# Kernel tuning notes

Hardware: AMD Instinct MI355X
Metric: run time of the kernel (lower is better)

Reference implementation:

```python
import jax, jax.numpy as jnp
import numpy as np

B, N, D, H, HID, EN = 2, 4096, 128, 4, 32, 16
ALPHA = 0.2           # LeakyReLU slope
NEG = -9e15           # masked_fill value from the original code


def setup_inputs() -> dict:
    key = jax.random.key(0)
    ks = jax.random.split(key, 6)
    fea = jax.random.normal(ks[0], (B, N, D), dtype=jnp.float32)
    # binary dense adjacency (regulon x gene), square here so narrow() is identity
    adj = jax.random.randint(ks[1], (B, N, N), 0, 2).astype(jnp.float32)
    # per-head GAT params (xavier-ish scale)
    W_heads = jax.random.normal(ks[2], (H, D, HID), dtype=jnp.float32) * 0.1
    a_heads = jax.random.normal(ks[3], (H, 2 * HID, 1), dtype=jnp.float32) * 0.1
    W_last = jax.random.normal(ks[4], (H * HID, EN), dtype=jnp.float32) * 0.1
    a_last = jax.random.normal(ks[5], (2 * EN, 1), dtype=jnp.float32) * 0.1
    return {"fea_mats": fea, "adj_mats": adj, "W_heads": W_heads,
            "a_heads": a_heads, "W_last": W_last, "a_last": a_last}


def _gat_layer(x, adj, W, a, concat):
    # x: [N, d_in], adj: [nr, N], W: [d_in, out], a: [2*out, 1]
    out_dim = W.shape[1]
    wh = x @ W                                   # [N, out]
    nr = adj.shape[0]
    wh1 = wh[:nr] @ a[:out_dim]                  # [nr, 1]
    wh2 = wh @ a[out_dim:]                       # [N, 1]
    e = jax.nn.leaky_relu(wh1 + wh2.T, ALPHA)    # [nr, N]
    # _prepare_attentions: mask by adj, weight by adj, fill zeros with -9e15
    att = jnp.where(adj != 0, e * adj, 0.0)
    att = jnp.where(att == 0, NEG, att)
    att = jax.nn.softmax(att, axis=1)
    # the original detaches attention via a numpy roundtrip
    att = jax.lax.stop_gradient(att)
    res = att @ wh                               # [nr, out]
    return jax.nn.elu(res) if concat else res


def reference(fea_mats, adj_mats, W_heads, a_heads, W_last, a_last):
    def per_sample(x, adj):
        # multi-head attention layers (concat=True), vmapped over heads
        heads = jax.vmap(lambda W, a: _gat_layer(x, adj, W, a, True))(W_heads, a_heads)  # [H, N, HID]
        xcat = jnp.transpose(heads, (1, 0, 2)).reshape(x.shape[0], H * HID)  # torch.cat(dim=1)
        nr = adj.shape[0]
        out = _gat_layer(xcat, adj[:, :nr], W_last, a_last, False)  # adj.narrow(1,0,nr)
        return jax.nn.elu(out)  # [N, EN]
    return jax.vmap(per_sample)(fea_mats, adj_mats)  # [B, N, EN]
```

## Files before the change

### kernel.cpp

```cpp
#include <hip/hip_runtime.h>
#include <hip/hip_bf16.h>
#include <stdint.h>

#define B_ 2
#define N_ 4096
#define D_ 128
#define H_ 4
#define HID_ 32
#define EN_ 16
#define ALPHA_ 0.2f
#define S1_ 4
#define S2_ 4
#define LOG2E_ 1.4426950408889634f

typedef __attribute__((ext_vector_type(8))) _Float16 f16x8;
typedef __attribute__((ext_vector_type(4))) float f32x4;
typedef __attribute__((ext_vector_type(8))) unsigned short u16x8;

__device__ __forceinline__ unsigned short f2h(float v) {
    _Float16 h = (_Float16)v;
    return *(unsigned short*)&h;
}

__global__ __launch_bounds__(256) void prep_kernel(
    const float* __restrict__ adj, unsigned long long* __restrict__ mask,
    const float* __restrict__ fea, const float* __restrict__ Wh,
    const float* __restrict__ a_heads,
    float* __restrict__ wh1, float* __restrict__ wh2,
    float* __restrict__ cmax1, unsigned short* __restrict__ whTt)
{
    __shared__ float xs[32][132];
    __shared__ float WT[32][132];
    __shared__ float Wa[2][128];
    __shared__ float as_[2 * HID_];
    __shared__ unsigned short ts[32][32];
    __shared__ float rmax[32];
    const int tid = threadIdx.x;

    if (blockIdx.x < 2048) {
        const int b = blockIdx.x >> 10, ib = blockIdx.x & 1023;
        const int i = ib * 4 + (tid >> 6);
        const int lane = tid & 63;
        const float* ar = adj + ((size_t)b * N_ + i) * N_;
        unsigned long long* mrow = mask + ((size_t)b * N_ + i) * 64;
#pragma unroll 4
        for (int c = 0; c < 16; ++c) {
            float4 v = *(const float4*)(ar + c * 256 + lane * 4);
            unsigned long long b0 = __ballot(v.x != 0.f);
            unsigned long long b1 = __ballot(v.y != 0.f);
            unsigned long long b2 = __ballot(v.z != 0.f);
            unsigned long long b3 = __ballot(v.w != 0.f);
            if (lane == 0) {
                ulonglong2 w01 = {b0, b1}, w23 = {b2, b3};
                *(ulonglong2*)(mrow + c * 4) = w01;
                *(ulonglong2*)(mrow + c * 4 + 2) = w23;
            }
        }
        return;
    }
    const int l0 = blockIdx.x - 2048;
    const int ib = l0 & 127, h = (l0 >> 7) & 3, b = l0 >> 9;
    const int i0 = ib * 32;
    const float* Wp = Wh + (size_t)h * D_ * HID_;
    for (int l = tid; l < 1024; l += 256) {
        float4 w4 = *(const float4*)(Wp + l * 4);
        int k = l >> 3, d = (l & 7) * 4;
        WT[d][k] = w4.x; WT[d + 1][k] = w4.y; WT[d + 2][k] = w4.z; WT[d + 3][k] = w4.w;
    }
    if (tid < 2 * HID_) as_[tid] = a_heads[h * 2 * HID_ + tid];
    const float* xp = fea + ((size_t)b * N_ + i0) * D_;
    for (int l = tid; l < 1024; l += 256) {
        int r = l >> 5, k4 = (l & 31) * 4;
        *(float4*)&xs[r][k4] = *(const float4*)(xp + r * D_ + k4);
    }
    __syncthreads();
    {
        const int k = tid & 127, j = tid >> 7;
        const float* wr = Wp + k * HID_;
        const float* aw = &as_[j * HID_];
        float s = 0.f;
#pragma unroll
        for (int d = 0; d < HID_; d += 4) {
            float4 w4 = *(const float4*)(wr + d);
            s += w4.x * aw[d] + w4.y * aw[d + 1] + w4.z * aw[d + 2] + w4.w * aw[d + 3];
        }
        Wa[j][k] = s;
    }
    const int c = tid & 15, rg = (tid >> 4) * 2;
    float a0[2] = {0.f, 0.f}, a1[2] = {0.f, 0.f};
#pragma unroll 8
    for (int k = 0; k < D_; k += 4) {
        float4 w0 = *(float4*)&WT[c][k];
        float4 w1 = *(float4*)&WT[c + 16][k];
#pragma unroll
        for (int i = 0; i < 2; ++i) {
            float4 x4 = *(float4*)&xs[rg + i][k];
            a0[i] += x4.x * w0.x + x4.y * w0.y + x4.z * w0.z + x4.w * w0.w;
            a1[i] += x4.x * w1.x + x4.y * w1.y + x4.z * w1.z + x4.w * w1.w;
        }
    }
#pragma unroll
    for (int i = 0; i < 2; ++i) {
        ts[c][rg + i] = f2h(a0[i]);
        ts[c + 16][rg + i] = f2h(a1[i]);
    }
    __syncthreads();
    {
        const int row = tid >> 3, q = tid & 7;
        float d1 = 0.f, d2 = 0.f;
#pragma unroll
        for (int k = q * 16; k < q * 16 + 16; k += 4) {
            float4 x4 = *(float4*)&xs[row][k];
            float4 u = *(float4*)&Wa[0][k];
            float4 v = *(float4*)&Wa[1][k];
            d1 += x4.x * u.x + x4.y * u.y + x4.z * u.z + x4.w * u.w;
            d2 += x4.x * v.x + x4.y * v.y + x4.z * v.z + x4.w * v.w;
        }
        d1 += __shfl_xor(d1, 1); d1 += __shfl_xor(d1, 2); d1 += __shfl_xor(d1, 4);
        d2 += __shfl_xor(d2, 1); d2 += __shfl_xor(d2, 2); d2 += __shfl_xor(d2, 4);
        if (q == 0) {
            const size_t o = (size_t)(b * H_ + h) * N_ + i0 + row;
            wh1[o] = d1 * LOG2E_;
            wh2[o] = d2 * LOG2E_;
            rmax[row] = d2 * LOG2E_;
        }
    }
    __syncthreads();
    if (tid < 128) {
        const int d = tid >> 2, part = (tid & 3) * 8;
        unsigned short* dst = whTt + ((size_t)(b * H_ + h) * 64 + (i0 >> 6)) * 2048
                            + d * 64 + (i0 & 63) + part;
        *(u16x8*)dst = *(u16x8*)&ts[d][part];
    }
    if (tid < 32) {
        float mx = rmax[tid];
#pragma unroll
        for (int off = 16; off; off >>= 1) mx = fmaxf(mx, __shfl_xor(mx, off));
        if (tid == 0) cmax1[(size_t)(b * H_ + h) * 128 + ib] = mx;
    }
}

__global__ __launch_bounds__(256) void attn1_kernel(
    const unsigned long long* __restrict__ mask, const unsigned short* __restrict__ whT,
    const float* __restrict__ wh1, const float* __restrict__ wh2,
    const float* __restrict__ cmax1,
    float* __restrict__ x2p, float* __restrict__ l1p)
{
    __shared__ unsigned long long mask_s[32][17];
    __shared__ float Btab[H_][2][1024];
    const int b = blockIdx.z, split = blockIdx.y, i0 = blockIdx.x * 32;
    const int tid = threadIdx.x, lane = tid & 63, h = tid >> 6;
    const int m = lane & 15, quad = lane >> 4;
    {
        const int r = tid >> 3, w = (tid & 7) * 2;
        ulonglong2 mw = *(const ulonglong2*)(mask + ((size_t)b * N_ + i0 + r) * 64
                                             + split * 16 + w);
        mask_s[r][w] = mw.x; mask_s[r][w + 1] = mw.y;
    }
    const float* cm = cmax1 + (size_t)(b * H_ + h) * 128;
    float Mh = fmaxf(cm[lane], cm[lane + 64]);
#pragma unroll
    for (int off = 32; off; off >>= 1) Mh = fmaxf(Mh, __shfl_xor(Mh, off));
    const size_t bhN = (size_t)(b * H_ + h) * N_;
    const float* w2g = wh2 + bhN + split * 1024;
#pragma unroll
    for (int g = 0; g < 4; ++g) {
        float4 v = *(const float4*)(w2g + g * 256 + lane * 4);
        float4 eb, ep;
        eb.x = __builtin_amdgcn_exp2f(v.x - Mh);
        eb.y = __builtin_amdgcn_exp2f(v.y - Mh);
        eb.z = __builtin_amdgcn_exp2f(v.z - Mh);
        eb.w = __builtin_amdgcn_exp2f(v.w - Mh);
        ep.x = __builtin_amdgcn_exp2f(ALPHA_ * (v.x - Mh));
        ep.y = __builtin_amdgcn_exp2f(ALPHA_ * (v.y - Mh));
        ep.z = __builtin_amdgcn_exp2f(ALPHA_ * (v.z - Mh));
        ep.w = __builtin_amdgcn_exp2f(ALPHA_ * (v.w - Mh));
        *(float4*)&Btab[h][0][g * 256 + lane * 4] = eb;
        *(float4*)&Btab[h][1][g * 256 + lane * 4] = ep;
    }
    const float w1r0 = wh1[bhN + i0 + m];
    const float w1r1 = wh1[bhN + i0 + 16 + m];
    const float sb0 = w1r0 + Mh, sb1 = w1r1 + Mh;
    const float mr0 = fmaxf(sb0, ALPHA_ * sb0);
    const float mr1 = fmaxf(sb1, ALPHA_ * sb1);
    const float th0 = -w1r0, th1 = -w1r1;
    const float Fp0 = __builtin_amdgcn_exp2f(sb0 - mr0);
    const float Fn0 = __builtin_amdgcn_exp2f(ALPHA_ * sb0 - mr0);
    const float Fp1 = __builtin_amdgcn_exp2f(sb1 - mr1);
    const float Fn1 = __builtin_amdgcn_exp2f(ALPHA_ * sb1 - mr1);
    const float* wvb = wh2 + bhN + split * 1024 + quad * 8;
    const unsigned short* bpb = whT + (size_t)(b * H_ + h) * 131072
                              + (size_t)split * 16 * 2048 + m * 64 + quad * 8;
    f32x4 a00 = {0.f,0.f,0.f,0.f}, a01 = {0.f,0.f,0.f,0.f}, a02 = {0.f,0.f,0.f,0.f};
    f32x4 a10 = {0.f,0.f,0.f,0.f}, a11 = {0.f,0.f,0.f,0.f}, a12 = {0.f,0.f,0.f,0.f};
    f16x8 ones;
#pragma unroll
    for (int q = 0; q < 8; ++q) ones[q] = (_Float16)1.0f;
    __syncthreads();

    for (int c = 0; c < 4; ++c) {
#pragma unroll
        for (int q4 = 0; q4 < 4; ++q4) {
            const int t = c * 4 + q4;
            const int half = q4 >> 1;
            unsigned int pw0, pw1, pw2, pw3, qw0, qw1, qw2, qw3;
            pw0 = ((const unsigned int*)&mask_s[m][c*4+0])[half];
            pw1 = ((const unsigned int*)&mask_s[m][c*4+1])[half];
            pw2 = ((const unsigned int*)&mask_s[m][c*4+2])[half];
            pw3 = ((const unsigned int*)&mask_s[m][c*4+3])[half];
            qw0 = ((const unsigned int*)&mask_s[m+16][c*4+0])[half];
            qw1 = ((const unsigned int*)&mask_s[m+16][c*4+1])[half];
            qw2 = ((const unsigned int*)&mask_s[m+16][c*4+2])[half];
            qw3 = ((const unsigned int*)&mask_s[m+16][c*4+3])[half];
            const unsigned short* bp = bpb + (size_t)t * 2048;
            const float* nw = wvb + t * 64;
#pragma unroll
            for (int ks = 0; ks < 2; ++ks) {
                f16x8 bb0 = *(const f16x8*)(bp + ks * 32);
                f16x8 bb1 = *(const f16x8*)(bp + 1024 + ks * 32);
                float wv8[8];
                *(float4*)&wv8[0] = *(const float4*)(nw + ks * 32);
                *(float4*)&wv8[4] = *(const float4*)(nw + ks * 32 + 4);
                float Bj[8], Bp8[8];
                {
                    const float* Bb = &Btab[h][0][t * 64 + ks * 32 + quad * 8];
                    const float* Pb = &Btab[h][1][t * 64 + ks * 32 + quad * 8];
                    *(float4*)&Bj[0]  = *(const float4*)Bb;
                    *(float4*)&Bj[4]  = *(const float4*)(Bb + 4);
                    *(float4*)&Bp8[0] = *(const float4*)Pb;
                    *(float4*)&Bp8[4] = *(const float4*)(Pb + 4);
                }
                const int sh = ((16 * q4 + 8 * ks) & 31) + 2 * quad;
                const unsigned int gp0 = (pw0 >> sh) & 3u;
                const unsigned int gp1 = (pw1 >> sh) & 3u;
                const unsigned int gp2 = (pw2 >> sh) & 3u;
                const unsigned int gp3 = (pw3 >> sh) & 3u;
                const unsigned int gq0 = (qw0 >> sh) & 3u;
                const unsigned int gq1 = (qw1 >> sh) & 3u;
                const unsigned int gq2 = (qw2 >> sh) & 3u;
                const unsigned int gq3 = (qw3 >> sh) & 3u;
                f16x8 af0, af1;
#pragma unroll
                for (int qq = 0; qq < 4; ++qq) {
                    float r0p[2], r1p[2];
#pragma unroll
                    for (int cc = 0; cc < 2; ++cc) {
                        const int jj = qq * 2 + cc;
                        const unsigned int bsel = 1u << (jj >> 2);
                        const unsigned int gp = (jj&3)==0?gp0:(jj&3)==1?gp1:(jj&3)==2?gp2:gp3;
                        const unsigned int gq = (jj&3)==0?gq0:(jj&3)==1?gq1:(jj&3)==2?gq2:gq3;
                        const float w2v = wv8[jj];
                        float v0s = (w2v > th0) ? Fp0 * Bj[jj] : Fn0 * Bp8[jj];
                        r0p[cc] = ((gp & bsel) == 0u || w2v == th0) ? 0.f : v0s;
                        float v1s = (w2v > th1) ? Fp1 * Bj[jj] : Fn1 * Bp8[jj];
                        r1p[cc] = ((gq & bsel) == 0u || w2v == th1) ? 0.f : v1s;
                    }
                    auto pr0 = __builtin_amdgcn_cvt_pkrtz(r0p[0], r0p[1]);
                    af0[qq*2] = (_Float16)pr0[0]; af0[qq*2+1] = (_Float16)pr0[1];
                    auto pr1 = __builtin_amdgcn_cvt_pkrtz(r1p[0], r1p[1]);
                    af1[qq*2] = (_Float16)pr1[0]; af1[qq*2+1] = (_Float16)pr1[1];
                }
                a00 = __builtin_amdgcn_mfma_f32_16x16x32_f16(af0, bb0, a00, 0, 0, 0);
                a01 = __builtin_amdgcn_mfma_f32_16x16x32_f16(af0, bb1, a01, 0, 0, 0);
                a02 = __builtin_amdgcn_mfma_f32_16x16x32_f16(af0, ones, a02, 0, 0, 0);
                a10 = __builtin_amdgcn_mfma_f32_16x16x32_f16(af1, bb0, a10, 0, 0, 0);
                a11 = __builtin_amdgcn_mfma_f32_16x16x32_f16(af1, bb1, a11, 0, 0, 0);
                a12 = __builtin_amdgcn_mfma_f32_16x16x32_f16(af1, ones, a12, 0, 0, 0);
            }
        }
    }
    float* xp = x2p + (((size_t)split * B_ + b) * N_ + i0) * D_ + h * HID_;
#pragma unroll
    for (int reg = 0; reg < 4; ++reg) {
        const int row = quad * 4 + reg;
        xp[(size_t)row * D_ + m] = a00[reg];
        xp[(size_t)row * D_ + 16 + m] = a01[reg];
        xp[(size_t)(row + 16) * D_ + m] = a10[reg];
        xp[(size_t)(row + 16) * D_ + 16 + m] = a11[reg];
    }
    if (m == 0) {
        float* lp = l1p + (((size_t)split * B_ + b) * N_ + i0) * H_ + h;
#pragma unroll
        for (int reg = 0; reg < 4; ++reg) {
            lp[(size_t)(quad * 4 + reg) * H_] = a02[reg];
            lp[(size_t)(quad * 4 + reg + 16) * H_] = a12[reg];
        }
    }
}

__global__ __launch_bounds__(256) void proj2_kernel(
    const float* __restrict__ x2p, const float* __restrict__ l1p,
    const float* __restrict__ Wl, const float* __restrict__ a_last,
    float* __restrict__ wh1b, float* __restrict__ wh2b,
    float* __restrict__ cmax2, unsigned short* __restrict__ whT2t)
{
    __shared__ float Ws[D_ * EN_];
    __shared__ float xs[16][D_];
    __shared__ float as_[2 * EN_];
    __shared__ unsigned short ts[EN_][16];
    __shared__ float rmax[16];
    const int b = blockIdx.y, i0 = blockIdx.x * 16, tid = threadIdx.x;
    for (int idx = tid * 4; idx < D_ * EN_; idx += 1024)
        *(float4*)&Ws[idx] = *(const float4*)(Wl + idx);
    if (tid < 2 * EN_) as_[tid] = a_last[tid];
    for (int idx = tid * 4; idx < 16 * D_; idx += 1024) {
        const int r = idx >> 7, hd = idx & 127, h = hd >> 5;
        float4 v = {0.f, 0.f, 0.f, 0.f};
        float l = 0.f;
#pragma unroll
        for (int s = 0; s < S1_; ++s) {
            const size_t gi = ((size_t)s * B_ + b) * N_ + i0 + r;
            float4 p = *(const float4*)(x2p + gi * D_ + hd);
            v.x += p.x; v.y += p.y; v.z += p.z; v.w += p.w;
            l += l1p[gi * H_ + h];
        }
        float linv = 1.f / fmaxf(l, 1e-30f);
        float o0 = v.x * linv, o1 = v.y * linv, o2 = v.z * linv, o3 = v.w * linv;
        xs[r][hd]     = o0 > 0.f ? o0 : expm1f(o0);
        xs[r][hd + 1] = o1 > 0.f ? o1 : expm1f(o1);
        xs[r][hd + 2] = o2 > 0.f ? o2 : expm1f(o2);
        xs[r][hd + 3] = o3 > 0.f ? o3 : expm1f(o3);
    }
    __syncthreads();
    const int r = tid >> 4, e = tid & 15;
    float acc = 0.f;
#pragma unroll 8
    for (int k = 0; k < D_; ++k) acc += xs[r][k] * Ws[k * EN_ + e];
    ts[e][r] = f2h(acc);
    float d1 = acc * as_[e], d2 = acc * as_[EN_ + e];
#pragma unroll
    for (int off = 8; off; off >>= 1) {
        d1 += __shfl_xor(d1, off);
        d2 += __shfl_xor(d2, off);
    }
    d1 *= LOG2E_; d2 *= LOG2E_;
    if (e == 0) {
        wh1b[(size_t)b * N_ + i0 + r] = d1;
        wh2b[(size_t)b * N_ + i0 + r] = d2;
        rmax[r] = d2;
    }
    __syncthreads();
    if (tid < EN_) {
        unsigned short* dst = whT2t + (size_t)b * 65536
                            + (i0 >> 6) * 1024 + tid * 64 + (i0 & 63);
        *(u16x8*)dst = *(u16x8*)&ts[tid][0];
        *(u16x8*)(dst + 8) = *(u16x8*)&ts[tid][8];
    }
    if (tid == 0) {
        float mx = rmax[0];
#pragma unroll
        for (int k = 1; k < 16; ++k) mx = fmaxf(mx, rmax[k]);
        cmax2[(size_t)b * 256 + blockIdx.x] = mx;
    }
}

__global__ __launch_bounds__(256) void attn2_kernel(
    const unsigned long long* __restrict__ mask, const unsigned short* __restrict__ whT2,
    const float* __restrict__ wh1b, const float* __restrict__ wh2b,
    const float* __restrict__ cmax2,
    float* __restrict__ outp, float* __restrict__ outlp)
{
    __shared__ unsigned long long mask_s[32][17];
    __shared__ float accred[4][32][17];
    __shared__ float lred[4][32];
    __shared__ float Btab2[2][1024];
    const int b = blockIdx.z, split = blockIdx.y, i0 = blockIdx.x * 32;
    const int tid = threadIdx.x, lane = tid & 63, wv = tid >> 6;
    const int m = lane & 15, quad = lane >> 4;
    {
        const int r = tid >> 3, w = (tid & 7) * 2;
        ulonglong2 mw = *(const ulonglong2*)(mask + ((size_t)b * N_ + i0 + r) * 64
                                             + split * 16 + w);
        mask_s[r][w] = mw.x; mask_s[r][w + 1] = mw.y;
    }
    const float* cm = cmax2 + (size_t)b * 256;
    float4 c0 = *(const float4*)(cm + lane * 4);
    float Mh = fmaxf(fmaxf(c0.x, c0.y), fmaxf(c0.z, c0.w));
#pragma unroll
    for (int off = 32; off; off >>= 1) Mh = fmaxf(Mh, __shfl_xor(Mh, off));
    {
        float4 v = *(const float4*)(wh2b + (size_t)b * N_ + split * 1024 + tid * 4);
        float4 eb, ep;
        eb.x = __builtin_amdgcn_exp2f(v.x - Mh);
        eb.y = __builtin_amdgcn_exp2f(v.y - Mh);
        eb.z = __builtin_amdgcn_exp2f(v.z - Mh);
        eb.w = __builtin_amdgcn_exp2f(v.w - Mh);
        ep.x = __builtin_amdgcn_exp2f(ALPHA_ * (v.x - Mh));
        ep.y = __builtin_amdgcn_exp2f(ALPHA_ * (v.y - Mh));
        ep.z = __builtin_amdgcn_exp2f(ALPHA_ * (v.z - Mh));
        ep.w = __builtin_amdgcn_exp2f(ALPHA_ * (v.w - Mh));
        *(float4*)&Btab2[0][tid * 4] = eb;
        *(float4*)&Btab2[1][tid * 4] = ep;
    }
    const float w1r0 = wh1b[(size_t)b * N_ + i0 + m];
    const float w1r1 = wh1b[(size_t)b * N_ + i0 + 16 + m];
    const float sb0 = w1r0 + Mh, sb1 = w1r1 + Mh;
    const float mr0 = fmaxf(sb0, ALPHA_ * sb0);
    const float mr1 = fmaxf(sb1, ALPHA_ * sb1);
    const float th0 = -w1r0, th1 = -w1r1;
    const float Fp0 = __builtin_amdgcn_exp2f(sb0 - mr0);
    const float Fn0 = __builtin_amdgcn_exp2f(ALPHA_ * sb0 - mr0);
    const float Fp1 = __builtin_amdgcn_exp2f(sb1 - mr1);
    const float Fn1 = __builtin_amdgcn_exp2f(ALPHA_ * sb1 - mr1);
    const unsigned short* wTb = whT2 + (size_t)b * 65536
                              + (size_t)(split * 16 + wv * 4) * 1024 + m * 64 + quad * 8;
    const float* wvb = wh2b + (size_t)b * N_ + split * 1024 + wv * 256 + quad * 8;
    f32x4 a0 = {0.f,0.f,0.f,0.f}, a1 = {0.f,0.f,0.f,0.f};
    f32x4 l0 = {0.f,0.f,0.f,0.f}, l1 = {0.f,0.f,0.f,0.f};
    f16x8 ones;
#pragma unroll
    for (int q = 0; q < 8; ++q) ones[q] = (_Float16)1.0f;
    __syncthreads();
#pragma unroll
    for (int q4 = 0; q4 < 4; ++q4) {
        const int half = q4 >> 1;
        unsigned int pw0, pw1, pw2, pw3, qw0, qw1, qw2, qw3;
        pw0 = ((const unsigned int*)&mask_s[m][wv*4+0])[half];
        pw1 = ((const unsigned int*)&mask_s[m][wv*4+1])[half];
        pw2 = ((const unsigned int*)&mask_s[m][wv*4+2])[half];
        pw3 = ((const unsigned int*)&mask_s[m][wv*4+3])[half];
        qw0 = ((const unsigned int*)&mask_s[m+16][wv*4+0])[half];
        qw1 = ((const unsigned int*)&mask_s[m+16][wv*4+1])[half];
        qw2 = ((const unsigned int*)&mask_s[m+16][wv*4+2])[half];
        qw3 = ((const unsigned int*)&mask_s[m+16][wv*4+3])[half];
        const unsigned short* bp = wTb + (size_t)q4 * 1024;
        const float* nw = wvb + q4 * 64;
#pragma unroll
        for (int ks = 0; ks < 2; ++ks) {
            f16x8 bb = *(const f16x8*)(bp + ks * 32);
            float wv8[8];
            *(float4*)&wv8[0] = *(const float4*)(nw + ks * 32);
            *(float4*)&wv8[4] = *(const float4*)(nw + ks * 32 + 4);
            float Bj[8], Bp8[8];
            {
                const float* Bb = &Btab2[0][wv * 256 + q4 * 64 + ks * 32 + quad * 8];
                const float* Pb = &Btab2[1][wv * 256 + q4 * 64 + ks * 32 + quad * 8];
                *(float4*)&Bj[0]  = *(const float4*)Bb;
                *(float4*)&Bj[4]  = *(const float4*)(Bb + 4);
                *(float4*)&Bp8[0] = *(const float4*)Pb;
                *(float4*)&Bp8[4] = *(const float4*)(Pb + 4);
            }
            const int sh = ((16 * q4 + 8 * ks) & 31) + 2 * quad;
            const unsigned int gp0 = (pw0 >> sh) & 3u;
            const unsigned int gp1 = (pw1 >> sh) & 3u;
            const unsigned int gp2 = (pw2 >> sh) & 3u;
            const unsigned int gp3 = (pw3 >> sh) & 3u;
            const unsigned int gq0 = (qw0 >> sh) & 3u;
            const unsigned int gq1 = (qw1 >> sh) & 3u;
            const unsigned int gq2 = (qw2 >> sh) & 3u;
            const unsigned int gq3 = (qw3 >> sh) & 3u;
            f16x8 af0, af1;
#pragma unroll
            for (int qq = 0; qq < 4; ++qq) {
                float r0p[2], r1p[2];
#pragma unroll
                for (int cc = 0; cc < 2; ++cc) {
                    const int jj = qq * 2 + cc;
                    const unsigned int bsel = 1u << (jj >> 2);
                    const unsigned int gp = (jj&3)==0?gp0:(jj&3)==1?gp1:(jj&3)==2?gp2:gp3;
                    const unsigned int gq = (jj&3)==0?gq0:(jj&3)==1?gq1:(jj&3)==2?gq2:gq3;
                    const float w2v = wv8[jj];
                    float v0s = (w2v > th0) ? Fp0 * Bj[jj] : Fn0 * Bp8[jj];
                    r0p[cc] = ((gp & bsel) == 0u || w2v == th0) ? 0.f : v0s;
                    float v1s = (w2v > th1) ? Fp1 * Bj[jj] : Fn1 * Bp8[jj];
                    r1p[cc] = ((gq & bsel) == 0u || w2v == th1) ? 0.f : v1s;
                }
                auto pr0 = __builtin_amdgcn_cvt_pkrtz(r0p[0], r0p[1]);
                af0[qq*2] = (_Float16)pr0[0]; af0[qq*2+1] = (_Float16)pr0[1];
                auto pr1 = __builtin_amdgcn_cvt_pkrtz(r1p[0], r1p[1]);
                af1[qq*2] = (_Float16)pr1[0]; af1[qq*2+1] = (_Float16)pr1[1];
            }
            a0 = __builtin_amdgcn_mfma_f32_16x16x32_f16(af0, bb, a0, 0, 0, 0);
            l0 = __builtin_amdgcn_mfma_f32_16x16x32_f16(af0, ones, l0, 0, 0, 0);
            a1 = __builtin_amdgcn_mfma_f32_16x16x32_f16(af1, bb, a1, 0, 0, 0);
            l1 = __builtin_amdgcn_mfma_f32_16x16x32_f16(af1, ones, l1, 0, 0, 0);
        }
    }
#pragma unroll
    for (int reg = 0; reg < 4; ++reg) {
        accred[wv][quad * 4 + reg][m] = a0[reg];
        accred[wv][quad * 4 + reg + 16][m] = a1[reg];
    }
    if (m == 0) {
#pragma unroll
        for (int reg = 0; reg < 4; ++reg) {
            lred[wv][quad * 4 + reg] = l0[reg];
            lred[wv][quad * 4 + reg + 16] = l1[reg];
        }
    }
    __syncthreads();
    const int row = tid >> 4, col = tid & 15;
    float s0 = accred[0][row][col] + accred[1][row][col]
             + accred[2][row][col] + accred[3][row][col];
    float s1 = accred[0][row + 16][col] + accred[1][row + 16][col]
             + accred[2][row + 16][col] + accred[3][row + 16][col];
    float* op = outp + (((size_t)split * B_ + b) * N_ + i0) * EN_;
    op[(size_t)row * EN_ + col] = s0;
    op[(size_t)(row + 16) * EN_ + col] = s1;
    if (tid < 32) {
        float l = lred[0][tid] + lred[1][tid] + lred[2][tid] + lred[3][tid];
        outlp[((size_t)split * B_ + b) * N_ + i0 + tid] = l;
    }
}

__global__ __launch_bounds__(256) void finalize2_kernel(
    const float* __restrict__ outp, const float* __restrict__ outlp,
    float* __restrict__ out)
{
    const int id = blockIdx.x * 256 + threadIdx.x;
    const int gi = id >> 4;
    float num = 0.f, l = 0.f;
#pragma unroll
    for (int s = 0; s < S2_; ++s) {
        num += outp[(size_t)s * B_ * N_ * EN_ + id];
        l   += outlp[(size_t)s * B_ * N_ + gi];
    }
    float v = num / fmaxf(l, 1e-30f);
    out[id] = v > 0.f ? v : expm1f(v);
}

extern "C" void kernel_launch(void* const* d_in, const int* in_sizes, int n_in,
                              void* d_out, int out_size, void* d_ws, size_t ws_size,
                              hipStream_t stream)
{
    const float* fea = (const float*)d_in[0];
    const float* adj = (const float*)d_in[1];
    const float* Wh  = (const float*)d_in[2];
    const float* ah  = (const float*)d_in[3];
    const float* Wl  = (const float*)d_in[4];
    const float* al  = (const float*)d_in[5];

    float* p = (float*)d_ws;
    float* wh1   = p;  p += (size_t)B_ * H_ * N_;
    float* wh2   = p;  p += (size_t)B_ * H_ * N_;
    float* wh1b  = p;  p += (size_t)B_ * N_;
    float* wh2b  = p;  p += (size_t)B_ * N_;
    float* cmax1 = p;  p += (size_t)B_ * H_ * 128;
    float* cmax2 = p;  p += (size_t)B_ * 256;
    float* l1p   = p;  p += (size_t)S1_ * B_ * N_ * H_;
    float* x2p   = p;  p += (size_t)S1_ * B_ * N_ * D_;
    float* outp  = p;  p += (size_t)S2_ * B_ * N_ * EN_;
    float* outlp = p;  p += (size_t)S2_ * B_ * N_;
    unsigned long long* mask = (unsigned long long*)p;
    unsigned short* whTt  = (unsigned short*)(mask + (size_t)B_ * N_ * 64);
    unsigned short* whT2t = whTt + (size_t)B_ * H_ * 131072;

    prep_kernel<<<2048 + B_ * H_ * 128, 256, 0, stream>>>(adj, mask, fea, Wh, ah,
                                                          wh1, wh2, cmax1, whTt);
    attn1_kernel<<<dim3(N_ / 32, S1_, B_), 256, 0, stream>>>(mask, whTt, wh1, wh2, cmax1,
                                                             x2p, l1p);
    proj2_kernel<<<dim3(N_ / 16, B_), 256, 0, stream>>>(x2p, l1p, Wl, al,
                                                        wh1b, wh2b, cmax2, whT2t);
    attn2_kernel<<<dim3(N_ / 32, S2_, B_), 256, 0, stream>>>(mask, whT2t, wh1b, wh2b, cmax2,
                                                             outp, outlp);
    finalize2_kernel<<<(B_ * N_ * EN_) / 256, 256, 0, stream>>>(outp, outlp, (float*)d_out);
}
```

Before: 276.3 us.

## Split attn1 across heads in grid; waves split key range with LDS reduction

attn1 now launches one block per (batch, head) with its four waves each covering a quarter of the key tiles for the same head, instead of one wave per head looping over all tiles. Partial MFMA accumulators and row sums are reduced through shared memory and written with vectorized float4 stores. Shared memory is aliased in both attention kernels to shrink the LDS footprint, with an added barrier before reuse. This gives four times more blocks and shorter per-wave loops, at the cost of reloading the mask per head and an extra LDS reduction step.

```diff
diff --git a/kernel.cpp b/kernel.cpp
--- a/kernel.cpp
+++ b/kernel.cpp
@@ -146,10 +146,14 @@
     const float* __restrict__ cmax1,
     float* __restrict__ x2p, float* __restrict__ l1p)
 {
-    __shared__ unsigned long long mask_s[32][17];
-    __shared__ float Btab[H_][2][1024];
-    const int b = blockIdx.z, split = blockIdx.y, i0 = blockIdx.x * 32;
-    const int tid = threadIdx.x, lane = tid & 63, h = tid >> 6;
+    __shared__ __align__(16) char smem[18944];
+    unsigned long long (*mask_s)[17] = (unsigned long long(*)[17])smem;
+    float (*Btab)[1024] = (float(*)[1024])(smem + 4352);
+    float (*accred)[32][36] = (float(*)[32][36])smem;
+    float (*lred)[32] = (float(*)[32])(smem + 18432);
+    const int bh = blockIdx.z, b = bh >> 2, h = bh & 3;
+    const int split = blockIdx.y, i0 = blockIdx.x * 32;
+    const int tid = threadIdx.x, lane = tid & 63, wv = tid >> 6;
     const int m = lane & 15, quad = lane >> 4;
     {
         const int r = tid >> 3, w = (tid & 7) * 2;
@@ -162,10 +166,8 @@
 #pragma unroll
     for (int off = 32; off; off >>= 1) Mh = fmaxf(Mh, __shfl_xor(Mh, off));
     const size_t bhN = (size_t)(b * H_ + h) * N_;
-    const float* w2g = wh2 + bhN + split * 1024;
-#pragma unroll
-    for (int g = 0; g < 4; ++g) {
-        float4 v = *(const float4*)(w2g + g * 256 + lane * 4);
+    {
+        float4 v = *(const float4*)(wh2 + bhN + split * 1024 + tid * 4);
         float4 eb, ep;
         eb.x = __builtin_amdgcn_exp2f(v.x - Mh);
         eb.y = __builtin_amdgcn_exp2f(v.y - Mh);
@@ -175,8 +177,8 @@
         ep.y = __builtin_amdgcn_exp2f(ALPHA_ * (v.y - Mh));
         ep.z = __builtin_amdgcn_exp2f(ALPHA_ * (v.z - Mh));
         ep.w = __builtin_amdgcn_exp2f(ALPHA_ * (v.w - Mh));
-        *(float4*)&Btab[h][0][g * 256 + lane * 4] = eb;
-        *(float4*)&Btab[h][1][g * 256 + lane * 4] = ep;
+        *(float4*)&Btab[0][tid * 4] = eb;
+        *(float4*)&Btab[1][tid * 4] = ep;
     }
     const float w1r0 = wh1[bhN + i0 + m];
     const float w1r1 = wh1[bhN + i0 + 16 + m];
@@ -198,93 +200,108 @@
     for (int q = 0; q < 8; ++q) ones[q] = (_Float16)1.0f;
     __syncthreads();
 
-    for (int c = 0; c < 4; ++c) {
-#pragma unroll
-        for (int q4 = 0; q4 < 4; ++q4) {
-            const int t = c * 4 + q4;
-            const int half = q4 >> 1;
-            unsigned int pw0, pw1, pw2, pw3, qw0, qw1, qw2, qw3;
-            pw0 = ((const unsigned int*)&mask_s[m][c*4+0])[half];
-            pw1 = ((const unsigned int*)&mask_s[m][c*4+1])[half];
-            pw2 = ((const unsigned int*)&mask_s[m][c*4+2])[half];
-            pw3 = ((const unsigned int*)&mask_s[m][c*4+3])[half];
-            qw0 = ((const unsigned int*)&mask_s[m+16][c*4+0])[half];
-            qw1 = ((const unsigned int*)&mask_s[m+16][c*4+1])[half];
-            qw2 = ((const unsigned int*)&mask_s[m+16][c*4+2])[half];
-            qw3 = ((const unsigned int*)&mask_s[m+16][c*4+3])[half];
-            const unsigned short* bp = bpb + (size_t)t * 2048;
-            const float* nw = wvb + t * 64;
-#pragma unroll
-            for (int ks = 0; ks < 2; ++ks) {
-                f16x8 bb0 = *(const f16x8*)(bp + ks * 32);
-                f16x8 bb1 = *(const f16x8*)(bp + 1024 + ks * 32);
-                float wv8[8];
-                *(float4*)&wv8[0] = *(const float4*)(nw + ks * 32);
-                *(float4*)&wv8[4] = *(const float4*)(nw + ks * 32 + 4);
-                float Bj[8], Bp8[8];
-                {
-                    const float* Bb = &Btab[h][0][t * 64 + ks * 32 + quad * 8];
-                    const float* Pb = &Btab[h][1][t * 64 + ks * 32 + quad * 8];
-                    *(float4*)&Bj[0]  = *(const float4*)Bb;
-                    *(float4*)&Bj[4]  = *(const float4*)(Bb + 4);
-                    *(float4*)&Bp8[0] = *(const float4*)Pb;
-                    *(float4*)&Bp8[4] = *(const float4*)(Pb + 4);
+#pragma unroll
+    for (int q4 = 0; q4 < 4; ++q4) {
+        const int t = wv * 4 + q4;
+        const int half = q4 >> 1;
+        unsigned int pw0, pw1, pw2, pw3, qw0, qw1, qw2, qw3;
+        pw0 = ((const unsigned int*)&mask_s[m][wv*4+0])[half];
+        pw1 = ((const unsigned int*)&mask_s[m][wv*4+1])[half];
+        pw2 = ((const unsigned int*)&mask_s[m][wv*4+2])[half];
+        pw3 = ((const unsigned int*)&mask_s[m][wv*4+3])[half];
+        qw0 = ((const unsigned int*)&mask_s[m+16][wv*4+0])[half];
+        qw1 = ((const unsigned int*)&mask_s[m+16][wv*4+1])[half];
+        qw2 = ((const unsigned int*)&mask_s[m+16][wv*4+2])[half];
+        qw3 = ((const unsigned int*)&mask_s[m+16][wv*4+3])[half];
+        const unsigned short* bp = bpb + (size_t)t * 2048;
+        const float* nw = wvb + t * 64;
+#pragma unroll
+        for (int ks = 0; ks < 2; ++ks) {
+            f16x8 bb0 = *(const f16x8*)(bp + ks * 32);
+            f16x8 bb1 = *(const f16x8*)(bp + 1024 + ks * 32);
+            float wv8[8];
+            *(float4*)&wv8[0] = *(const float4*)(nw + ks * 32);
+            *(float4*)&wv8[4] = *(const float4*)(nw + ks * 32 + 4);
+            float Bj[8], Bp8[8];
+            {
+                const float* Bb = &Btab[0][t * 64 + ks * 32 + quad * 8];
+                const float* Pb = &Btab[1][t * 64 + ks * 32 + quad * 8];
+                *(float4*)&Bj[0]  = *(const float4*)Bb;
+                *(float4*)&Bj[4]  = *(const float4*)(Bb + 4);
+                *(float4*)&Bp8[0] = *(const float4*)Pb;
+                *(float4*)&Bp8[4] = *(const float4*)(Pb + 4);
+            }
+            const int sh = ((16 * q4 + 8 * ks) & 31) + 2 * quad;
+            const unsigned int gp0 = (pw0 >> sh) & 3u;
+            const unsigned int gp1 = (pw1 >> sh) & 3u;
+            const unsigned int gp2 = (pw2 >> sh) & 3u;
+            const unsigned int gp3 = (pw3 >> sh) & 3u;
+            const unsigned int gq0 = (qw0 >> sh) & 3u;
+            const unsigned int gq1 = (qw1 >> sh) & 3u;
+            const unsigned int gq2 = (qw2 >> sh) & 3u;
+            const unsigned int gq3 = (qw3 >> sh) & 3u;
+            f16x8 af0, af1;
+#pragma unroll
+            for (int qq = 0; qq < 4; ++qq) {
+                float r0p[2], r1p[2];
+#pragma unroll
+                for (int cc = 0; cc < 2; ++cc) {
+                    const int jj = qq * 2 + cc;
+                    const unsigned int bsel = 1u << (jj >> 2);
+                    const unsigned int gp = (jj&3)==0?gp0:(jj&3)==1?gp1:(jj&3)==2?gp2:gp3;
+                    const unsigned int gq = (jj&3)==0?gq0:(jj&3)==1?gq1:(jj&3)==2?gq2:gq3;
+                    const float w2v = wv8[jj];
+                    float v0s = (w2v > th0) ? Fp0 * Bj[jj] : Fn0 * Bp8[jj];
+                    r0p[cc] = ((gp & bsel) == 0u || w2v == th0) ? 0.f : v0s;
+                    float v1s = (w2v > th1) ? Fp1 * Bj[jj] : Fn1 * Bp8[jj];
+                    r1p[cc] = ((gq & bsel) == 0u || w2v == th1) ? 0.f : v1s;
                 }
-                const int sh = ((16 * q4 + 8 * ks) & 31) + 2 * quad;
-                const unsigned int gp0 = (pw0 >> sh) & 3u;
-                const unsigned int gp1 = (pw1 >> sh) & 3u;
-                const unsigned int gp2 = (pw2 >> sh) & 3u;
-                const unsigned int gp3 = (pw3 >> sh) & 3u;
-                const unsigned int gq0 = (qw0 >> sh) & 3u;
-                const unsigned int gq1 = (qw1 >> sh) & 3u;
-                const unsigned int gq2 = (qw2 >> sh) & 3u;
-                const unsigned int gq3 = (qw3 >> sh) & 3u;
-                f16x8 af0, af1;
-#pragma unroll
-                for (int qq = 0; qq < 4; ++qq) {
-                    float r0p[2], r1p[2];
-#pragma unroll
-                    for (int cc = 0; cc < 2; ++cc) {
-                        const int jj = qq * 2 + cc;
-                        const unsigned int bsel = 1u << (jj >> 2);
-                        const unsigned int gp = (jj&3)==0?gp0:(jj&3)==1?gp1:(jj&3)==2?gp2:gp3;
-                        const unsigned int gq = (jj&3)==0?gq0:(jj&3)==1?gq1:(jj&3)==2?gq2:gq3;
-                        const float w2v = wv8[jj];
-                        float v0s = (w2v > th0) ? Fp0 * Bj[jj] : Fn0 * Bp8[jj];
-                        r0p[cc] = ((gp & bsel) == 0u || w2v == th0) ? 0.f : v0s;
-                        float v1s = (w2v > th1) ? Fp1 * Bj[jj] : Fn1 * Bp8[jj];
-                        r1p[cc] = ((gq & bsel) == 0u || w2v == th1) ? 0.f : v1s;
-                    }
-                    auto pr0 = __builtin_amdgcn_cvt_pkrtz(r0p[0], r0p[1]);
-                    af0[qq*2] = (_Float16)pr0[0]; af0[qq*2+1] = (_Float16)pr0[1];
-                    auto pr1 = __builtin_amdgcn_cvt_pkrtz(r1p[0], r1p[1]);
-                    af1[qq*2] = (_Float16)pr1[0]; af1[qq*2+1] = (_Float16)pr1[1];
-                }
-                a00 = __builtin_amdgcn_mfma_f32_16x16x32_f16(af0, bb0, a00, 0, 0, 0);
-                a01 = __builtin_amdgcn_mfma_f32_16x16x32_f16(af0, bb1, a01, 0, 0, 0);
-                a02 = __builtin_amdgcn_mfma_f32_16x16x32_f16(af0, ones, a02, 0, 0, 0);
-                a10 = __builtin_amdgcn_mfma_f32_16x16x32_f16(af1, bb0, a10, 0, 0, 0);
-                a11 = __builtin_amdgcn_mfma_f32_16x16x32_f16(af1, bb1, a11, 0, 0, 0);
-                a12 = __builtin_amdgcn_mfma_f32_16x16x32_f16(af1, ones, a12, 0, 0, 0);
+                auto pr0 = __builtin_amdgcn_cvt_pkrtz(r0p[0], r0p[1]);
+                af0[qq*2] = (_Float16)pr0[0]; af0[qq*2+1] = (_Float16)pr0[1];
+                auto pr1 = __builtin_amdgcn_cvt_pkrtz(r1p[0], r1p[1]);
+                af1[qq*2] = (_Float16)pr1[0]; af1[qq*2+1] = (_Float16)pr1[1];
             }
-        }
-    }
-    float* xp = x2p + (((size_t)split * B_ + b) * N_ + i0) * D_ + h * HID_;
+            a00 = __builtin_amdgcn_mfma_f32_16x16x32_f16(af0, bb0, a00, 0, 0, 0);
+            a01 = __builtin_amdgcn_mfma_f32_16x16x32_f16(af0, bb1, a01, 0, 0, 0);
+            a02 = __builtin_amdgcn_mfma_f32_16x16x32_f16(af0, ones, a02, 0, 0, 0);
+            a10 = __builtin_amdgcn_mfma_f32_16x16x32_f16(af1, bb0, a10, 0, 0, 0);
+            a11 = __builtin_amdgcn_mfma_f32_16x16x32_f16(af1, bb1, a11, 0, 0, 0);
+            a12 = __builtin_amdgcn_mfma_f32_16x16x32_f16(af1, ones, a12, 0, 0, 0);
+        }
+    }
+    __syncthreads();
 #pragma unroll
     for (int reg = 0; reg < 4; ++reg) {
-        const int row = quad * 4 + reg;
-        xp[(size_t)row * D_ + m] = a00[reg];
-        xp[(size_t)row * D_ + 16 + m] = a01[reg];
-        xp[(size_t)(row + 16) * D_ + m] = a10[reg];
-        xp[(size_t)(row + 16) * D_ + 16 + m] = a11[reg];
+        accred[wv][quad * 4 + reg][m]           = a00[reg];
+        accred[wv][quad * 4 + reg][m + 16]      = a01[reg];
+        accred[wv][quad * 4 + reg + 16][m]      = a10[reg];
+        accred[wv][quad * 4 + reg + 16][m + 16] = a11[reg];
     }
     if (m == 0) {
-        float* lp = l1p + (((size_t)split * B_ + b) * N_ + i0) * H_ + h;
 #pragma unroll
         for (int reg = 0; reg < 4; ++reg) {
-            lp[(size_t)(quad * 4 + reg) * H_] = a02[reg];
-            lp[(size_t)(quad * 4 + reg + 16) * H_] = a12[reg];
-        }
+            lred[wv][quad * 4 + reg]      = a02[reg];
+            lred[wv][quad * 4 + reg + 16] = a12[reg];
+        }
+    }
+    __syncthreads();
+    {
+        const int row = tid >> 3, c4 = (tid & 7) * 4;
+        float4 s0 = *(float4*)&accred[0][row][c4];
+        float4 s1 = *(float4*)&accred[1][row][c4];
+        float4 s2 = *(float4*)&accred[2][row][c4];
+        float4 s3 = *(float4*)&accred[3][row][c4];
+        float4 s;
+        s.x = s0.x + s1.x + s2.x + s3.x;
+        s.y = s0.y + s1.y + s2.y + s3.y;
+        s.z = s0.z + s1.z + s2.z + s3.z;
+        s.w = s0.w + s1.w + s2.w + s3.w;
+        float* xp = x2p + (((size_t)split * B_ + b) * N_ + i0) * D_ + h * HID_;
+        *(float4*)&xp[(size_t)row * D_ + c4] = s;
+    }
+    if (tid < 32) {
+        float l = lred[0][tid] + lred[1][tid] + lred[2][tid] + lred[3][tid];
+        l1p[(((size_t)split * B_ + b) * N_ + i0 + tid) * H_ + h] = l;
     }
 }
 
@@ -360,10 +377,11 @@
     const float* __restrict__ cmax2,
     float* __restrict__ outp, float* __restrict__ outlp)
 {
-    __shared__ unsigned long long mask_s[32][17];
-    __shared__ float accred[4][32][17];
-    __shared__ float lred[4][32];
-    __shared__ float Btab2[2][1024];
+    __shared__ __align__(16) char smem[12544];
+    unsigned long long (*mask_s)[17] = (unsigned long long(*)[17])smem;
+    float (*Btab2)[1024] = (float(*)[1024])(smem + 4352);
+    float (*accred)[32][17] = (float(*)[32][17])smem;
+    float (*lred)[32] = (float(*)[32])(smem + 8704);
     const int b = blockIdx.z, split = blockIdx.y, i0 = blockIdx.x * 32;
     const int tid = threadIdx.x, lane = tid & 63, wv = tid >> 6;
     const int m = lane & 15, quad = lane >> 4;
@@ -476,6 +494,7 @@
             l1 = __builtin_amdgcn_mfma_f32_16x16x32_f16(af1, ones, l1, 0, 0, 0);
         }
     }
+    __syncthreads();
 #pragma unroll
     for (int reg = 0; reg < 4; ++reg) {
         accred[wv][quad * 4 + reg][m] = a0[reg];
@@ -547,8 +566,8 @@
 
     prep_kernel<<<2048 + B_ * H_ * 128, 256, 0, stream>>>(adj, mask, fea, Wh, ah,
                                                           wh1, wh2, cmax1, whTt);
-    attn1_kernel<<<dim3(N_ / 32, S1_, B_), 256, 0, stream>>>(mask, whTt, wh1, wh2, cmax1,
-                                                             x2p, l1p);
+    attn1_kernel<<<dim3(N_ / 32, S1_, B_ * H_), 256, 0, stream>>>(mask, whTt, wh1, wh2,
+                                                                  cmax1, x2p, l1p);
     proj2_kernel<<<dim3(N_ / 16, B_), 256, 0, stream>>>(x2p, l1p, Wl, al,
                                                         wh1b, wh2b, cmax2, whT2t);
     attn2_kernel<<<dim3(N_ / 32, S2_, B_), 256, 0, stream>>>(mask, whT2t, wh1b, wh2b, cmax2,
```

Measured after the change: 277.5 us. No clear change (+0.4%).
